# Kernel optimization log

Measured on AMD Instinct MI355X. Metric: run time of the kernel, lower is better.

## Reference

```python
import jax, jax.numpy as jnp
import numpy as np

B, C, H, W = 8, 256, 128, 128
WS, NH = 8, 8
HD = C // NH
HID = 4 * C
EPS = 1e-5


def _dwconv(x, w, b, pad):
    # x: [B,C,H,W], w: [C,1,k,k] depthwise
    y = jax.lax.conv_general_dilated(
        x, w, window_strides=(1, 1), padding=[(pad, pad), (pad, pad)],
        feature_group_count=C, dimension_numbers=('NCHW', 'OIHW', 'NCHW'))
    return y + b[None, :, None, None]


def _ln(x, g, b):
    m = jnp.mean(x, axis=-1, keepdims=True)
    v = jnp.mean(jnp.square(x - m), axis=-1, keepdims=True)
    return (x - m) * jax.lax.rsqrt(v + EPS) * g + b


def _mha(x, wqkv, bqkv, wo, bo):
    # x: [N,L,C]; torch nn.MultiheadAttention with q=k=v=x
    N, L, _ = x.shape
    qkv = x @ wqkv.T + bqkv
    q, k, v = jnp.split(qkv, 3, axis=-1)
    q = q.reshape(N, L, NH, HD)
    k = k.reshape(N, L, NH, HD)
    v = v.reshape(N, L, NH, HD)
    scale = HD ** -0.5
    a = jnp.einsum('nqhd,nkhd->nhqk', q * scale, k)
    a = jax.nn.softmax(a, axis=-1)
    o = jnp.einsum('nhqk,nkhd->nqhd', a, v).reshape(N, L, C)
    return o @ wo.T + bo


def _window_partition(x):
    b, c, h, w = x.shape
    x = x.reshape(b, c, h // WS, WS, w // WS, WS)
    return jnp.transpose(x, (0, 2, 4, 3, 5, 1)).reshape(-1, WS, WS, c)


def _window_reverse(win, h, w):
    c = win.shape[-1]
    x = win.reshape(-1, h // WS, w // WS, WS, WS, c)
    return jnp.transpose(x, (0, 5, 1, 3, 2, 4)).reshape(-1, c, h, w)


def _grid_partition(x):
    b, c, h, w = x.shape
    x = x.reshape(b, c, WS, h // WS, WS, w // WS)
    return jnp.transpose(x, (0, 3, 5, 2, 4, 1)).reshape(-1, WS, WS, c)


def _grid_reverse(grid, h, w):
    c = grid.shape[-1]
    x = grid.reshape(-1, h // WS, w // WS, WS, WS, c)
    return jnp.transpose(x, (0, 5, 2, 1, 3, 4)).reshape(-1, c, h, w)


def setup_inputs() -> dict:
    key = jax.random.key(0)
    ks = jax.random.split(key, 32)
    n = lambda k, s, sc=0.02: jax.random.normal(k, s, jnp.float32) * sc
    z = lambda s: jnp.zeros(s, jnp.float32)
    return {
        'x': jax.random.normal(ks[0], (B, C, H, W), jnp.float32),
        'w1': n(ks[1], (C, 1, 3, 3)), 'b1': z((C,)),
        'w2': n(ks[2], (C, 1, 5, 5)), 'b2': z((C,)),
        'w3': n(ks[3], (C, 1, 7, 7)), 'b3': z((C,)),
        'wf': n(ks[4], (C, 3 * C)), 'bf': z((C,)),
        'gw': jnp.ones((C,), jnp.float32), 'bw': z((C,)),
        'wqkv_w': n(ks[5], (3 * C, C)), 'bqkv_w': z((3 * C,)),
        'wo_w': n(ks[6], (C, C)), 'bo_w': z((C,)),
        'gg': jnp.ones((C,), jnp.float32), 'bg': z((C,)),
        'wqkv_g': n(ks[7], (3 * C, C)), 'bqkv_g': z((3 * C,)),
        'wo_g': n(ks[8], (C, C)), 'bo_g': z((C,)),
        'gm': jnp.ones((C,), jnp.float32), 'bm': z((C,)),
        'm1w': n(ks[9], (HID, C)), 'm1b': z((HID,)),
        'm2w': n(ks[10], (C, HID)), 'm2b': z((C,)),
    }


def reference(x, w1, b1, w2, b2, w3, b3, wf, bf, gw, bw, wqkv_w, bqkv_w, wo_w, bo_w,
              gg, bg, wqkv_g, bqkv_g, wo_g, bo_g, gm, bm, m1w, m1b, m2w, m2b):
    s1 = _dwconv(x, w1, b1, 1)
    s2 = _dwconv(x, w2, b2, 2)
    s3 = _dwconv(x, w3, b3, 3)
    cat = jnp.concatenate([s1, s2, s3], axis=1)  # [B,3C,H,W]
    x_multi = jnp.einsum('bkhw,ck->bchw', cat, wf) + bf[None, :, None, None]

    # window attention branch
    xw = _window_partition(x_multi).reshape(-1, WS * WS, C)
    xw = _ln(xw, gw, bw)
    xw = _mha(xw, wqkv_w, bqkv_w, wo_w, bo_w).reshape(-1, WS, WS, C)
    x = x + _window_reverse(xw, H, W)

    # grid attention branch
    xg = _grid_partition(x).reshape(-1, WS * WS, C)
    xg = _ln(xg, gg, bg)
    xg = _mha(xg, wqkv_g, bqkv_g, wo_g, bo_g).reshape(-1, WS, WS, C)
    x = x + _grid_reverse(xg, H, W)

    # MLP over flattened tokens
    xf = x.reshape(B, C, H * W).transpose(0, 2, 1)  # [B,HW,C]
    h = _ln(xf, gm, bm)
    h = jax.nn.gelu(h @ m1w.T + m1b, approximate=False)
    h = h @ m2w.T + m2b
    xf = xf + h
    return xf.transpose(0, 2, 1).reshape(B, C, H, W)
```

## Files before the change

### kernel.cpp

```cpp
#include <hip/hip_runtime.h>
#include <hip/hip_bf16.h>
#include <math.h>


#define CC 256
#define HH 128
#define WW 128
#define HWSZ 16384

typedef __attribute__((ext_vector_type(8))) short short8v;
typedef __attribute__((ext_vector_type(4))) float float4v;

#if defined(__has_builtin)
#if __has_builtin(__builtin_amdgcn_global_load_lds)
#define USE_GLDS 1
#endif
#endif
#ifndef USE_GLDS
#define USE_GLDS 0
#endif

static __device__ __forceinline__ float bf2f(unsigned short u) {
    union { float f; unsigned int i; } x; x.i = ((unsigned int)u) << 16; return x.f;
}
static __device__ __forceinline__ unsigned short f2bf(float f) {
    union { float f; unsigned int i; } x; x.f = f;
    unsigned int r = x.i + 0x7FFFu + ((x.i >> 16) & 1u);
    return (unsigned short)(r >> 16);
}
template<int FMT> static __device__ __forceinline__ float ldin(const void* p, size_t i) {
    if (FMT == 0) return bf2f(((const unsigned short*)p)[i]);
    return ((const float*)p)[i];
}

#if USE_GLDS
static __device__ __forceinline__ void gload16(const unsigned short* g, unsigned short* l) {
    __builtin_amdgcn_global_load_lds(
        (const __attribute__((address_space(1))) unsigned int*)g,
        (__attribute__((address_space(3))) unsigned int*)l, 16, 0, 0);
}
#endif

__global__ void probe_kernel(const unsigned short* x, int* flags) {
    __shared__ int mx[256];
    int m = 0;
    for (int i = threadIdx.x; i < 65536; i += 256) {
        int e = (x[i] >> 7) & 0xFF;
        m = m > e ? m : e;
    }
    mx[threadIdx.x] = m; __syncthreads();
    for (int s = 128; s > 0; s >>= 1) {
        if (threadIdx.x < s) mx[threadIdx.x] = mx[threadIdx.x] > mx[threadIdx.x + s] ? mx[threadIdx.x] : mx[threadIdx.x + s];
        __syncthreads();
    }
    if (threadIdx.x == 0) flags[0] = (mx[0] > 200) ? 1 : 0;
}
__global__ void report_ws_kernel(unsigned short* out, long long n, float code) {
    long long i = (long long)blockIdx.x * blockDim.x + threadIdx.x;
    const long long st = (long long)gridDim.x * blockDim.x;
    unsigned short c = f2bf(code);
    for (; i < n; i += st) out[i] = c;
}

#define WF_OFF   0
#define WQW_OFF  196608
#define WOW_OFF  393216
#define WQG_OFF  458752
#define WOG_OFF  655360
#define M1W_OFF  720896
#define M2W_OFF  983040
#define WTOT     1245184
#define BF_OFF   0
#define GW_OFF   256
#define BW_OFF   512
#define BQW_OFF  768
#define BOW_OFF  1536
#define GG_OFF   1792
#define BG_OFF   2048
#define BQG_OFF  2304
#define BOG_OFF  3072
#define GM_OFF   3328
#define BM_OFF   3584
#define M1B_OFF  3840
#define M2B_OFF  4864
#define BTOT     5120

template<int FMT>
__global__ __launch_bounds__(256) void convert_weights_kernel(
    const void* __restrict__ wf, const void* __restrict__ wqkv_w, const void* __restrict__ wo_w,
    const void* __restrict__ wqkv_g, const void* __restrict__ wo_g,
    const void* __restrict__ m1w, const void* __restrict__ m2w,
    unsigned short* __restrict__ out, const int* __restrict__ flags)
{
    if (flags[0] != FMT) return;
    int i = blockIdx.x * 256 + threadIdx.x;
    const int st = gridDim.x * 256;
    for (; i < WTOT; i += st) {
        const void* src; int off;
        if (i < WQW_OFF)      { src = wf;     off = i; }
        else if (i < WOW_OFF) { src = wqkv_w; off = i - WQW_OFF; }
        else if (i < WQG_OFF) { src = wo_w;   off = i - WOW_OFF; }
        else if (i < WOG_OFF) { src = wqkv_g; off = i - WQG_OFF; }
        else if (i < M1W_OFF) { src = wo_g;   off = i - WOG_OFF; }
        else if (i < M2W_OFF) { src = m1w;    off = i - M1W_OFF; }
        else                  { src = m2w;    off = i - M2W_OFF; }
        out[i] = (FMT == 0) ? ((const unsigned short*)src)[off]
                            : f2bf(((const float*)src)[off]);
    }
}

template<int FMT>
__global__ __launch_bounds__(256) void convert_bias_kernel(
    const void* bf_, const void* gw, const void* bw, const void* bqkv_w, const void* bo_w,
    const void* gg, const void* bg, const void* bqkv_g, const void* bo_g,
    const void* gm, const void* bm, const void* m1b, const void* m2b,
    float* __restrict__ out, const int* __restrict__ flags)
{
    if (flags[0] != FMT) return;
    int i = blockIdx.x * 256 + threadIdx.x;
    if (i >= BTOT) return;
    const void* src; int off;
    if (i < GW_OFF)        { src = bf_;    off = i; }
    else if (i < BW_OFF)   { src = gw;     off = i - GW_OFF; }
    else if (i < BQW_OFF)  { src = bw;     off = i - BW_OFF; }
    else if (i < BOW_OFF)  { src = bqkv_w; off = i - BQW_OFF; }
    else if (i < GG_OFF)   { src = bo_w;   off = i - BOW_OFF; }
    else if (i < BG_OFF)   { src = gg;     off = i - GG_OFF; }
    else if (i < BQG_OFF)  { src = bg;     off = i - BG_OFF; }
    else if (i < BOG_OFF)  { src = bqkv_g; off = i - BQG_OFF; }
    else if (i < GM_OFF)   { src = bo_g;   off = i - BOG_OFF; }
    else if (i < BM_OFF)   { src = gm;     off = i - GM_OFF; }
    else if (i < M1B_OFF)  { src = bm;     off = i - BM_OFF; }
    else if (i < M2B_OFF)  { src = m1b;    off = i - M1B_OFF; }
    else                   { src = m2b;    off = i - M2B_OFF; }
    out[i] = ldin<FMT>(src, off);
}

template<int FMT>
__global__ __launch_bounds__(256) void transpose_in_kernel(
    const void* __restrict__ in, float* __restrict__ out, const int* __restrict__ flags)
{
    if (flags[0] != FMT) return;
    __shared__ float tile[64][65];
    const int b  = blockIdx.z;
    const int s0 = blockIdx.x * 64;
    const int r0 = blockIdx.y * 64;
    const int tx = threadIdx.x & 63;
    const int ty = threadIdx.x >> 6;
    const size_t sb = (size_t)b * CC * HWSZ;
    float* dst = out + (size_t)b * HWSZ * CC;
#pragma unroll
    for (int rr = 0; rr < 16; ++rr) {
        int row = ty + rr * 4;
        tile[row][tx] = ldin<FMT>(in, sb + (size_t)(r0 + row) * HWSZ + s0 + tx);
    }
    __syncthreads();
#pragma unroll
    for (int rr = 0; rr < 16; ++rr) {
        int srow = ty + rr * 4;
        dst[(size_t)(s0 + srow) * CC + r0 + tx] = tile[tx][srow];
    }
}

template<int FMT>
__global__ __launch_bounds__(256) void transpose_out_kernel(
    const float* __restrict__ in, void* __restrict__ out, const int* __restrict__ flags)
{
    if (flags[0] != FMT) return;
    __shared__ float tile[64][65];
    const int b  = blockIdx.z;
    const int h0 = blockIdx.x * 64;
    const int c0 = blockIdx.y * 64;
    const int tx = threadIdx.x & 63;
    const int ty = threadIdx.x >> 6;
    const float* src = in + (size_t)b * HWSZ * CC;
    const size_t db = (size_t)b * CC * HWSZ;
#pragma unroll
    for (int rr = 0; rr < 16; ++rr) {
        int row = ty + rr * 4;
        tile[row][tx] = src[(size_t)(h0 + row) * CC + c0 + tx];
    }
    __syncthreads();
#pragma unroll
    for (int rr = 0; rr < 16; ++rr) {
        int crow = ty + rr * 4;
        size_t di = db + (size_t)(c0 + crow) * HWSZ + h0 + tx;
        float v = tile[tx][crow];
        if (FMT) ((float*)out)[di] = v;
        else ((unsigned short*)out)[di] = f2bf(v);
    }
}

template<int FMT>
__global__ __launch_bounds__(256) void dwconv_cat_kernel(
    const void* __restrict__ x,
    const void* __restrict__ w1, const void* __restrict__ b1,
    const void* __restrict__ w2, const void* __restrict__ b2,
    const void* __restrict__ w3, const void* __restrict__ b3,
    unsigned short* __restrict__ cat, int Mc, const int* __restrict__ flags)
{
    if (flags[0] != FMT) return;
    __shared__ float patch[8][136];
    __shared__ float wt[83];
    const int hb = blockIdx.x;
    const int c  = blockIdx.y;
    const int b  = blockIdx.z;
    const int tid = threadIdx.x;

    if (tid < 83) {
        float v;
        if (tid < 9)       v = ldin<FMT>(w1, c * 9 + tid);
        else if (tid < 34) v = ldin<FMT>(w2, c * 25 + (tid - 9));
        else               v = ldin<FMT>(w3, c * 49 + (tid - 34));
        wt[tid] = v;
    }
    const int h0 = hb * 2;
    const size_t xb = ((size_t)b * CC + c) * HWSZ;
    for (int i = tid; i < 8 * 136; i += 256) {
        int r = i / 136, col = i % 136;
        int gh = h0 - 3 + r, gw = col - 3;
        float v = 0.f;
        if (gh >= 0 && gh < HH && gw >= 0 && gw < WW) v = ldin<FMT>(x, xb + gh * WW + gw);
        patch[r][col] = v;
    }
    __syncthreads();

    const int w  = tid & 127;
    const int dh = tid >> 7;
    const int pr = dh + 3;
    float s1 = ldin<FMT>(b1, c), s2 = ldin<FMT>(b2, c), s3 = ldin<FMT>(b3, c);
#pragma unroll
    for (int dy = -1; dy <= 1; ++dy)
#pragma unroll
        for (int dx = -1; dx <= 1; ++dx)
            s1 += patch[pr + dy][w + 3 + dx] * wt[(dy + 1) * 3 + (dx + 1)];
#pragma unroll
    for (int dy = -2; dy <= 2; ++dy)
#pragma unroll
        for (int dx = -2; dx <= 2; ++dx)
            s2 += patch[pr + dy][w + 3 + dx] * wt[9 + (dy + 2) * 5 + (dx + 2)];
#pragma unroll
    for (int dy = -3; dy <= 3; ++dy)
#pragma unroll
        for (int dx = -3; dx <= 3; ++dx)
            s3 += patch[pr + dy][w + 3 + dx] * wt[34 + (dy + 3) * 7 + (dx + 3)];

    const size_t m = (size_t)b * HWSZ + (size_t)(h0 + dh) * WW + w;
    cat[(size_t)c * Mc + m]         = f2bf(s1);
    cat[(size_t)(256 + c) * Mc + m] = f2bf(s2);
    cat[(size_t)(512 + c) * Mc + m] = f2bf(s3);
}

template<int ALAYOUT, int EPI>
__global__ __launch_bounds__(256) void gemm_mfma_kernel(
    const unsigned short* __restrict__ A, const unsigned short* __restrict__ Bw,
    const float* __restrict__ bias, void* __restrict__ Cout,
    int N, int K, int lda)
{
    constexpr int ASTR = ALAYOUT ? 72 : 64;
    __shared__ unsigned short As[128 * ASTR];
    __shared__ unsigned short Bs[128 * 64];
    const int tid  = threadIdx.x;
    const int lane = tid & 63;
    const int wv   = tid >> 6;
    const int wm   = (wv >> 1) * 64;
    const int wn   = (wv & 1) * 64;
    const int l15  = lane & 15;
    const int quad = lane >> 4;

    const int nbx = gridDim.x;
    const int nwg = nbx * gridDim.y;
    const int bid = blockIdx.y * nbx + blockIdx.x;
    const int swz = (bid & 7) * (nwg >> 3) + (bid >> 3);
    const int m0 = (swz / nbx) * 128;
    const int n0 = (swz % nbx) * 128;

    const int sr   = lane >> 3;
    const int scol = (lane & 7) * 8;

    float4v acc[4][4] = {};

    for (int k0 = 0; k0 < K; k0 += 64) {
        __syncthreads();
        if (ALAYOUT == 0) {
            const unsigned short* ga = A + (size_t)(m0 + wv * 32 + sr) * K + k0 + scol;
#pragma unroll
            for (int p = 0; p < 4; ++p) {
                unsigned short* lb = &As[(wv * 32 + p * 8) * 64];
#if USE_GLDS
                gload16(ga + (size_t)(p * 8) * K, lb);
#else
                *(short8v*)(lb + lane * 8) = *(const short8v*)(ga + (size_t)(p * 8) * K);
#endif
            }
        } else {
#pragma unroll
            for (int p = 0; p < 4; ++p) {
                const int k  = p * 16 + (tid >> 4);
                const int mm = (tid & 15) * 8;
                const unsigned short* g = A + (size_t)(k0 + k) * lda + m0 + mm;
                ushort4 va = *(const ushort4*)g;
                ushort4 vb = *(const ushort4*)(g + 4);
                As[(mm + 0) * 72 + k] = va.x; As[(mm + 1) * 72 + k] = va.y;
                As[(mm + 2) * 72 + k] = va.z; As[(mm + 3) * 72 + k] = va.w;
                As[(mm + 4) * 72 + k] = vb.x; As[(mm + 5) * 72 + k] = vb.y;
                As[(mm + 6) * 72 + k] = vb.z; As[(mm + 7) * 72 + k] = vb.w;
            }
        }
        {
            const unsigned short* gb = Bw + (size_t)(n0 + wv * 32 + sr) * K + k0 + scol;
#pragma unroll
            for (int p = 0; p < 4; ++p) {
                unsigned short* lb = &Bs[(wv * 32 + p * 8) * 64];
#if USE_GLDS
                gload16(gb + (size_t)(p * 8) * K, lb);
#else
                *(short8v*)(lb + lane * 8) = *(const short8v*)(gb + (size_t)(p * 8) * K);
#endif
            }
        }
#if USE_GLDS
        asm volatile("s_waitcnt vmcnt(0)" ::: "memory");
#endif
        __syncthreads();

#pragma unroll
        for (int ks = 0; ks < 64; ks += 32) {
            short8v af[4], bfv[4];
#pragma unroll
            for (int i = 0; i < 4; ++i)
                af[i] = *(const short8v*)&As[(wm + i * 16 + l15) * ASTR + ks + quad * 8];
#pragma unroll
            for (int i = 0; i < 4; ++i)
                bfv[i] = *(const short8v*)&Bs[(wn + i * 16 + l15) * 64 + ks + quad * 8];
#pragma unroll
            for (int mi = 0; mi < 4; ++mi)
#pragma unroll
                for (int ni = 0; ni < 4; ++ni)
                    acc[mi][ni] = __builtin_amdgcn_mfma_f32_16x16x32_bf16(
                        af[mi], bfv[ni], acc[mi][ni], 0, 0, 0);
        }
    }

    float bv[4];
#pragma unroll
    for (int ni = 0; ni < 4; ++ni) bv[ni] = bias[n0 + wn + ni * 16 + l15];

#pragma unroll
    for (int mi = 0; mi < 4; ++mi) {
#pragma unroll
        for (int r = 0; r < 4; ++r) {
            const size_t row = (size_t)(m0 + wm + mi * 16 + quad * 4 + r);
#pragma unroll
            for (int ni = 0; ni < 4; ++ni) {
                const int col = n0 + wn + ni * 16 + l15;
                float v = acc[mi][ni][r] + bv[ni];
                if (EPI == 0) {
                    ((unsigned short*)Cout)[row * N + col] = f2bf(v);
                } else if (EPI == 1) {
                    float g = 0.5f * v * (1.0f + erff(v * 0.70710678118654752f));
                    ((unsigned short*)Cout)[row * N + col] = f2bf(g);
                } else {
                    ((float*)Cout)[row * N + col] += v;
                }
            }
        }
    }
}

template<int FIN>
__global__ __launch_bounds__(256) void ln_kernel(
    const void* __restrict__ inv, const float* __restrict__ g,
    const float* __restrict__ b, unsigned short* __restrict__ out)
{
    const int lane = threadIdx.x & 63;
    const int wv   = threadIdx.x >> 6;
    const size_t m = (size_t)blockIdx.x * 4 + wv;
    const int c0 = lane * 4;
    float v[4];
    if (FIN == 0) {
        ushort4 u = *(const ushort4*)((const unsigned short*)inv + m * CC + c0);
        v[0] = bf2f(u.x); v[1] = bf2f(u.y); v[2] = bf2f(u.z); v[3] = bf2f(u.w);
    } else {
        float4 f = *(const float4*)((const float*)inv + m * CC + c0);
        v[0] = f.x; v[1] = f.y; v[2] = f.z; v[3] = f.w;
    }
    float s  = v[0] + v[1] + v[2] + v[3];
    float sq = v[0]*v[0] + v[1]*v[1] + v[2]*v[2] + v[3]*v[3];
#pragma unroll
    for (int off = 32; off > 0; off >>= 1) {
        s  += __shfl_xor(s,  off);
        sq += __shfl_xor(sq, off);
    }
    const float mean = s * 0.00390625f;
    float var = sq * 0.00390625f - mean * mean;
    if (var < 0.f) var = 0.f;
    const float rs = rsqrtf(var + 1e-5f);
    ushort4 o;
    o.x = f2bf((v[0] - mean) * rs * g[c0 + 0] + b[c0 + 0]);
    o.y = f2bf((v[1] - mean) * rs * g[c0 + 1] + b[c0 + 1]);
    o.z = f2bf((v[2] - mean) * rs * g[c0 + 2] + b[c0 + 2]);
    o.w = f2bf((v[3] - mean) * rs * g[c0 + 3] + b[c0 + 3]);
    *(ushort4*)(out + m * CC + c0) = o;
}

template<int MODE>
__global__ __launch_bounds__(256) void attn_kernel(
    const unsigned short* __restrict__ qkv, unsigned short* __restrict__ attn_out)
{
    __shared__ float qs[64][36];
    __shared__ float ks[64][36];
    __shared__ float vs[64][36];
    __shared__ float S[64][68];
    const int tid = threadIdx.x;
    const int wi  = blockIdx.x;
    const int b   = wi >> 8;
    const int rem = wi & 255;
    const int i2  = rem >> 4;
    const int j2  = rem & 15;

    const int t  = tid >> 2;
    const int c8 = (tid & 3) * 8;
    const int p = t >> 3, qq = t & 7;
    int h_r, w_r, h_w, w_w;
    if (MODE == 0) {
        h_r = i2 * 8 + p;  w_r = j2 * 8 + qq;
        h_w = h_r;         w_w = w_r;
    } else {
        h_r = p * 16 + i2; w_r = qq * 16 + j2;
        h_w = j2 * 8 + (i2 >> 1);
        w_w = (i2 & 1) * 64 + p * 8 + qq;
    }
    const size_t gt_r = (size_t)b * HWSZ + (size_t)h_r * WW + w_r;
    const size_t gt_w = (size_t)b * HWSZ + (size_t)h_w * WW + w_w;

    const float scale = 0.17677669529663687f;
    const int ti = tid >> 4;
    const int tj = tid & 15;

    for (int head = 0; head < 8; ++head) {
        const unsigned short* base = qkv + gt_r * 768 + head * 32 + c8;
        ushort4 qa = *(const ushort4*)(base);
        ushort4 qb = *(const ushort4*)(base + 4);
        ushort4 ka = *(const ushort4*)(base + 256);
        ushort4 kb = *(const ushort4*)(base + 260);
        ushort4 va = *(const ushort4*)(base + 512);
        ushort4 vb = *(const ushort4*)(base + 516);
        qs[t][c8 + 0] = bf2f(qa.x) * scale; qs[t][c8 + 1] = bf2f(qa.y) * scale;
        qs[t][c8 + 2] = bf2f(qa.z) * scale; qs[t][c8 + 3] = bf2f(qa.w) * scale;
        qs[t][c8 + 4] = bf2f(qb.x) * scale; qs[t][c8 + 5] = bf2f(qb.y) * scale;
        qs[t][c8 + 6] = bf2f(qb.z) * scale; qs[t][c8 + 7] = bf2f(qb.w) * scale;
        ks[t][c8 + 0] = bf2f(ka.x); ks[t][c8 + 1] = bf2f(ka.y);
        ks[t][c8 + 2] = bf2f(ka.z); ks[t][c8 + 3] = bf2f(ka.w);
        ks[t][c8 + 4] = bf2f(kb.x); ks[t][c8 + 5] = bf2f(kb.y);
        ks[t][c8 + 6] = bf2f(kb.z); ks[t][c8 + 7] = bf2f(kb.w);
        vs[t][c8 + 0] = bf2f(va.x); vs[t][c8 + 1] = bf2f(va.y);
        vs[t][c8 + 2] = bf2f(va.z); vs[t][c8 + 3] = bf2f(va.w);
        vs[t][c8 + 4] = bf2f(vb.x); vs[t][c8 + 5] = bf2f(vb.y);
        vs[t][c8 + 6] = bf2f(vb.z); vs[t][c8 + 7] = bf2f(vb.w);
        __syncthreads();

        float sr[4][4] = {};
#pragma unroll 8
        for (int c = 0; c < 32; ++c) {
            float qv[4], kv[4];
#pragma unroll
            for (int i = 0; i < 4; ++i) qv[i] = qs[ti * 4 + i][c];
#pragma unroll
            for (int j = 0; j < 4; ++j) kv[j] = ks[tj * 4 + j][c];
#pragma unroll
            for (int i = 0; i < 4; ++i)
#pragma unroll
                for (int j = 0; j < 4; ++j)
                    sr[i][j] += qv[i] * kv[j];
        }
#pragma unroll
        for (int i = 0; i < 4; ++i)
#pragma unroll
            for (int j = 0; j < 4; ++j)
                S[ti * 4 + i][tj * 4 + j] = sr[i][j];
        __syncthreads();

        {
            const int r  = tid >> 2;
            const int s0 = (tid & 3) * 16;
            float mx = -1e30f;
#pragma unroll
            for (int j = 0; j < 16; ++j) mx = fmaxf(mx, S[r][s0 + j]);
            mx = fmaxf(mx, __shfl_xor(mx, 1));
            mx = fmaxf(mx, __shfl_xor(mx, 2));
            float sum = 0.f;
#pragma unroll
            for (int j = 0; j < 16; ++j) {
                float e = expf(S[r][s0 + j] - mx);
                S[r][s0 + j] = e;
                sum += e;
            }
            sum += __shfl_xor(sum, 1);
            sum += __shfl_xor(sum, 2);
            float inv = 1.f / sum;
#pragma unroll
            for (int j = 0; j < 16; ++j) S[r][s0 + j] *= inv;
        }
        __syncthreads();

        float ov[8] = {};
#pragma unroll 8
        for (int j = 0; j < 64; ++j) {
            float pv = S[t][j];
            const float4 v0 = *(const float4*)&vs[j][c8];
            const float4 v1 = *(const float4*)&vs[j][c8 + 4];
            ov[0] += pv * v0.x; ov[1] += pv * v0.y;
            ov[2] += pv * v0.z; ov[3] += pv * v0.w;
            ov[4] += pv * v1.x; ov[5] += pv * v1.y;
            ov[6] += pv * v1.z; ov[7] += pv * v1.w;
        }
        unsigned short* op = attn_out + gt_w * CC + head * 32 + c8;
        ushort4 o1, o2;
        o1.x = f2bf(ov[0]); o1.y = f2bf(ov[1]); o1.z = f2bf(ov[2]); o1.w = f2bf(ov[3]);
        o2.x = f2bf(ov[4]); o2.y = f2bf(ov[5]); o2.z = f2bf(ov[6]); o2.w = f2bf(ov[7]);
        *(ushort4*)op = o1;
        *(ushort4*)(op + 4) = o2;
        __syncthreads();
    }
}

extern "C" void kernel_launch(void* const* d_in, const int* in_sizes, int n_in,
                              void* d_out, int out_size, void* d_ws, size_t ws_size,
                              hipStream_t stream)
{
    const void* x      = d_in[0];
    const void* w1     = d_in[1];  const void* b1  = d_in[2];
    const void* w2     = d_in[3];  const void* b2  = d_in[4];
    const void* w3     = d_in[5];  const void* b3  = d_in[6];
    const void* wf     = d_in[7];  const void* bf_ = d_in[8];
    const void* gw     = d_in[9];  const void* bw  = d_in[10];
    const void* wqkv_w = d_in[11]; const void* bqkv_w = d_in[12];
    const void* wo_w   = d_in[13]; const void* bo_w   = d_in[14];
    const void* gg     = d_in[15]; const void* bg  = d_in[16];
    const void* wqkv_g = d_in[17]; const void* bqkv_g = d_in[18];
    const void* wo_g   = d_in[19]; const void* bo_g   = d_in[20];
    const void* gm     = d_in[21]; const void* bm  = d_in[22];
    const void* m1w    = d_in[23]; const void* m1b = d_in[24];
    const void* m2w    = d_in[25]; const void* m2b = d_in[26];

    const size_t MiB = 1048576ull;
    const long long nout = (long long)out_size;

    if (72 * MiB > ws_size) {
        float wsMiB = (float)(ws_size / MiB);
        if (wsMiB > 8192.f) wsMiB = 8192.f;
        report_ws_kernel<<<1024, 256, 0, stream>>>((unsigned short*)d_out, nout, 1024.f + wsMiB);
        return;
    }

    int nb = 8;
    while (nb > 1 && (size_t)nb * 64 * MiB + 8 * MiB > ws_size) nb >>= 1;
    const int nchunks = 8 / nb;
    const int Mc = nb * HWSZ;

    char* ws = (char*)d_ws;
    float*          xs   = (float*)ws;
    unsigned short* regA = (unsigned short*)(ws + (size_t)nb * 16 * MiB);
    unsigned short* xmat = (unsigned short*)(ws + (size_t)nb * 48 * MiB);
    unsigned short* xln  = (unsigned short*)(ws + (size_t)nb * 56 * MiB);
    int*            flags = (int*)(ws + (size_t)nb * 64 * MiB);
    unsigned short* wbf  = (unsigned short*)(ws + (size_t)nb * 64 * MiB + 1 * MiB);
    float*          bcv  = (float*)(ws + (size_t)nb * 64 * MiB + 4 * MiB);

    probe_kernel<<<1, 256, 0, stream>>>((const unsigned short*)x, flags);
    convert_weights_kernel<0><<<1024, 256, 0, stream>>>(wf, wqkv_w, wo_w, wqkv_g, wo_g, m1w, m2w, wbf, flags);
    convert_weights_kernel<1><<<1024, 256, 0, stream>>>(wf, wqkv_w, wo_w, wqkv_g, wo_g, m1w, m2w, wbf, flags);
    convert_bias_kernel<0><<<20, 256, 0, stream>>>(bf_, gw, bw, bqkv_w, bo_w, gg, bg, bqkv_g, bo_g, gm, bm, m1b, m2b, bcv, flags);
    convert_bias_kernel<1><<<20, 256, 0, stream>>>(bf_, gw, bw, bqkv_w, bo_w, gg, bg, bqkv_g, bo_g, gm, bm, m1b, m2b, bcv, flags);

    const int MB = Mc / 128;
    for (int c = 0; c < nchunks; ++c) {
        const size_t elemOff = (size_t)c * nb * CC * HWSZ;
        const void* xc0 = (const void*)((const unsigned short*)x + elemOff);
        const void* xc1 = (const void*)((const float*)x + elemOff);
        void* outc0 = (void*)((unsigned short*)d_out + elemOff);
        void* outc1 = (void*)((float*)d_out + elemOff);
        unsigned short* cat  = regA;
        unsigned short* qkvb = regA;
        unsigned short* h1   = regA;
        unsigned short* xm   = xmat;
        unsigned short* attn = xmat;

        transpose_in_kernel<0><<<dim3(256, 4, nb), 256, 0, stream>>>(xc0, xs, flags);
        transpose_in_kernel<1><<<dim3(256, 4, nb), 256, 0, stream>>>(xc1, xs, flags);

        dwconv_cat_kernel<0><<<dim3(64, 256, nb), 256, 0, stream>>>(xc0, w1, b1, w2, b2, w3, b3, cat, Mc, flags);
        dwconv_cat_kernel<1><<<dim3(64, 256, nb), 256, 0, stream>>>(xc1, w1, b1, w2, b2, w3, b3, cat, Mc, flags);

        gemm_mfma_kernel<1, 0><<<dim3(2, MB), 256, 0, stream>>>(cat, wbf + WF_OFF, bcv + BF_OFF, xm, 256, 768, Mc);

        ln_kernel<0><<<Mc / 4, 256, 0, stream>>>(xm, bcv + GW_OFF, bcv + BW_OFF, xln);
        gemm_mfma_kernel<0, 0><<<dim3(6, MB), 256, 0, stream>>>(xln, wbf + WQW_OFF, bcv + BQW_OFF, qkvb, 768, 256, 0);
        attn_kernel<0><<<nb * 256, 256, 0, stream>>>(qkvb, attn);
        gemm_mfma_kernel<0, 2><<<dim3(2, MB), 256, 0, stream>>>(attn, wbf + WOW_OFF, bcv + BOW_OFF, xs, 256, 256, 0);

        ln_kernel<1><<<Mc / 4, 256, 0, stream>>>(xs, bcv + GG_OFF, bcv + BG_OFF, xln);
        gemm_mfma_kernel<0, 0><<<dim3(6, MB), 256, 0, stream>>>(xln, wbf + WQG_OFF, bcv + BQG_OFF, qkvb, 768, 256, 0);
        attn_kernel<1><<<nb * 256, 256, 0, stream>>>(qkvb, attn);
        gemm_mfma_kernel<0, 2><<<dim3(2, MB), 256, 0, stream>>>(attn, wbf + WOG_OFF, bcv + BOG_OFF, xs, 256, 256, 0);

        ln_kernel<1><<<Mc / 4, 256, 0, stream>>>(xs, bcv + GM_OFF, bcv + BM_OFF, xln);
        gemm_mfma_kernel<0, 1><<<dim3(8, MB), 256, 0, stream>>>(xln, wbf + M1W_OFF, bcv + M1B_OFF, h1, 1024, 256, 0);
        gemm_mfma_kernel<0, 2><<<dim3(2, MB), 256, 0, stream>>>(h1, wbf + M2W_OFF, bcv + M2B_OFF, xs, 256, 1024, 0);

        transpose_out_kernel<0><<<dim3(256, 4, nb), 256, 0, stream>>>(xs, outc0, flags);
        transpose_out_kernel<1><<<dim3(256, 4, nb), 256, 0, stream>>>(xs, outc1, flags);
    }
}
```

Baseline: 2.103 ms.

## Use MFMA for window attention and enlarge depthwise-conv row tiles

The attention kernel moves from scalar fp32 dot products in LDS to bf16 MFMA 16x16x32 for both QK^T and PV. Softmax now runs in registers using cross-lane shuffles, and two heads are processed per 64-channel group load. The depthwise conv kernel now handles 8 rows per block instead of 2 and loads its halo patch with vectorized float4 reads, which cuts redundant halo traffic. The trade-off is that probabilities and V go through bf16 rounding, and the conv block uses more LDS.

Result: faster. 1.842 ms (-12.4%).

```diff
diff --git a/kernel.cpp b/kernel.cpp
--- a/kernel.cpp
+++ b/kernel.cpp
@@ -200,7 +200,7 @@
     unsigned short* __restrict__ cat, int Mc, const int* __restrict__ flags)
 {
     if (flags[0] != FMT) return;
-    __shared__ float patch[8][136];
+    __shared__ float patch[14][140];
     __shared__ float wt[83];
     const int hb = blockIdx.x;
     const int c  = blockIdx.y;
@@ -214,41 +214,65 @@
         else               v = ldin<FMT>(w3, c * 49 + (tid - 34));
         wt[tid] = v;
     }
-    const int h0 = hb * 2;
+    const int h0 = hb * 8;
     const size_t xb = ((size_t)b * CC + c) * HWSZ;
-    for (int i = tid; i < 8 * 136; i += 256) {
-        int r = i / 136, col = i % 136;
-        int gh = h0 - 3 + r, gw = col - 3;
+
+    for (int i = tid; i < 448; i += 256) {
+        const int r  = i >> 5;
+        const int c4 = (i & 31) * 4;
+        const int gh = h0 - 3 + r;
+        float4 vv;
+        if (gh >= 0 && gh < HH) {
+            if (FMT == 0) {
+                ushort4 u = *(const ushort4*)((const unsigned short*)x + xb + (size_t)gh * WW + c4);
+                vv.x = bf2f(u.x); vv.y = bf2f(u.y); vv.z = bf2f(u.z); vv.w = bf2f(u.w);
+            } else {
+                vv = *(const float4*)((const float*)x + xb + (size_t)gh * WW + c4);
+            }
+        } else { vv.x = vv.y = vv.z = vv.w = 0.f; }
+        *(float4*)&patch[r][c4 + 4] = vv;
+    }
+    for (int i = tid; i < 84; i += 256) {
+        const int r = i / 6, j = i % 6;
+        const int gh = h0 - 3 + r;
+        const int gw = (j < 3) ? (j - 3) : (125 + j);
         float v = 0.f;
-        if (gh >= 0 && gh < HH && gw >= 0 && gw < WW) v = ldin<FMT>(x, xb + gh * WW + gw);
-        patch[r][col] = v;
+        if (gh >= 0 && gh < HH && gw >= 0 && gw < WW)
+            v = ldin<FMT>(x, xb + (size_t)gh * WW + gw);
+        patch[r][gw + 4] = v;
     }
     __syncthreads();
 
     const int w  = tid & 127;
-    const int dh = tid >> 7;
-    const int pr = dh + 3;
-    float s1 = ldin<FMT>(b1, c), s2 = ldin<FMT>(b2, c), s3 = ldin<FMT>(b3, c);
-#pragma unroll
-    for (int dy = -1; dy <= 1; ++dy)
-#pragma unroll
-        for (int dx = -1; dx <= 1; ++dx)
-            s1 += patch[pr + dy][w + 3 + dx] * wt[(dy + 1) * 3 + (dx + 1)];
-#pragma unroll
-    for (int dy = -2; dy <= 2; ++dy)
-#pragma unroll
-        for (int dx = -2; dx <= 2; ++dx)
-            s2 += patch[pr + dy][w + 3 + dx] * wt[9 + (dy + 2) * 5 + (dx + 2)];
-#pragma unroll
-    for (int dy = -3; dy <= 3; ++dy)
-#pragma unroll
-        for (int dx = -3; dx <= 3; ++dx)
-            s3 += patch[pr + dy][w + 3 + dx] * wt[34 + (dy + 3) * 7 + (dx + 3)];
-
-    const size_t m = (size_t)b * HWSZ + (size_t)(h0 + dh) * WW + w;
-    cat[(size_t)c * Mc + m]         = f2bf(s1);
-    cat[(size_t)(256 + c) * Mc + m] = f2bf(s2);
-    cat[(size_t)(512 + c) * Mc + m] = f2bf(s3);
+    const int rb = (tid >> 7) * 4;
+    const float bb1 = ldin<FMT>(b1, c), bb2 = ldin<FMT>(b2, c), bb3 = ldin<FMT>(b3, c);
+
+#pragma unroll
+    for (int ri = 0; ri < 4; ++ri) {
+        const int row = rb + ri;
+        const int pr  = row + 3;
+        float s1 = bb1, s2 = bb2, s3 = bb3;
+#pragma unroll
+        for (int dy = -1; dy <= 1; ++dy)
+#pragma unroll
+            for (int dx = -1; dx <= 1; ++dx)
+                s1 += patch[pr + dy][w + 4 + dx] * wt[(dy + 1) * 3 + (dx + 1)];
+#pragma unroll
+        for (int dy = -2; dy <= 2; ++dy)
+#pragma unroll
+            for (int dx = -2; dx <= 2; ++dx)
+                s2 += patch[pr + dy][w + 4 + dx] * wt[9 + (dy + 2) * 5 + (dx + 2)];
+#pragma unroll
+        for (int dy = -3; dy <= 3; ++dy)
+#pragma unroll
+            for (int dx = -3; dx <= 3; ++dx)
+                s3 += patch[pr + dy][w + 4 + dx] * wt[34 + (dy + 3) * 7 + (dx + 3)];
+
+        const size_t m = (size_t)b * HWSZ + (size_t)(h0 + row) * WW + w;
+        cat[(size_t)c * Mc + m]         = f2bf(s1);
+        cat[(size_t)(256 + c) * Mc + m] = f2bf(s2);
+        cat[(size_t)(512 + c) * Mc + m] = f2bf(s3);
+    }
 }
 
 template<int ALAYOUT, int EPI>
@@ -408,120 +432,119 @@
 __global__ __launch_bounds__(256) void attn_kernel(
     const unsigned short* __restrict__ qkv, unsigned short* __restrict__ attn_out)
 {
-    __shared__ float qs[64][36];
-    __shared__ float ks[64][36];
-    __shared__ float vs[64][36];
-    __shared__ float S[64][68];
-    const int tid = threadIdx.x;
-    const int wi  = blockIdx.x;
-    const int b   = wi >> 8;
-    const int rem = wi & 255;
-    const int i2  = rem >> 4;
-    const int j2  = rem & 15;
-
-    const int t  = tid >> 2;
-    const int c8 = (tid & 3) * 8;
-    const int p = t >> 3, qq = t & 7;
-    int h_r, w_r, h_w, w_w;
-    if (MODE == 0) {
-        h_r = i2 * 8 + p;  w_r = j2 * 8 + qq;
-        h_w = h_r;         w_w = w_r;
-    } else {
-        h_r = p * 16 + i2; w_r = qq * 16 + j2;
-        h_w = j2 * 8 + (i2 >> 1);
-        w_w = (i2 & 1) * 64 + p * 8 + qq;
-    }
-    const size_t gt_r = (size_t)b * HWSZ + (size_t)h_r * WW + w_r;
-    const size_t gt_w = (size_t)b * HWSZ + (size_t)h_w * WW + w_w;
+    __shared__ unsigned short q_lds[64 * 72];
+    __shared__ unsigned short k_lds[64 * 72];
+    __shared__ unsigned short v_lds[64 * 72];
+    __shared__ unsigned short vt_lds[32 * 72];
+    __shared__ unsigned short p_lds[64 * 72];
+
+    const int tid  = threadIdx.x;
+    const int lane = tid & 63;
+    const int wv   = tid >> 6;
+    const int l15  = lane & 15;
+    const int quad = lane >> 4;
+    const int wi   = blockIdx.x;
+    const int b    = wi >> 8;
+    const int rem  = wi & 255;
+    const int i2   = rem >> 4;
+    const int j2   = rem & 15;
 
     const float scale = 0.17677669529663687f;
-    const int ti = tid >> 4;
-    const int tj = tid & 15;
-
-    for (int head = 0; head < 8; ++head) {
-        const unsigned short* base = qkv + gt_r * 768 + head * 32 + c8;
-        ushort4 qa = *(const ushort4*)(base);
-        ushort4 qb = *(const ushort4*)(base + 4);
-        ushort4 ka = *(const ushort4*)(base + 256);
-        ushort4 kb = *(const ushort4*)(base + 260);
-        ushort4 va = *(const ushort4*)(base + 512);
-        ushort4 vb = *(const ushort4*)(base + 516);
-        qs[t][c8 + 0] = bf2f(qa.x) * scale; qs[t][c8 + 1] = bf2f(qa.y) * scale;
-        qs[t][c8 + 2] = bf2f(qa.z) * scale; qs[t][c8 + 3] = bf2f(qa.w) * scale;
-        qs[t][c8 + 4] = bf2f(qb.x) * scale; qs[t][c8 + 5] = bf2f(qb.y) * scale;
-        qs[t][c8 + 6] = bf2f(qb.z) * scale; qs[t][c8 + 7] = bf2f(qb.w) * scale;
-        ks[t][c8 + 0] = bf2f(ka.x); ks[t][c8 + 1] = bf2f(ka.y);
-        ks[t][c8 + 2] = bf2f(ka.z); ks[t][c8 + 3] = bf2f(ka.w);
-        ks[t][c8 + 4] = bf2f(kb.x); ks[t][c8 + 5] = bf2f(kb.y);
-        ks[t][c8 + 6] = bf2f(kb.z); ks[t][c8 + 7] = bf2f(kb.w);
-        vs[t][c8 + 0] = bf2f(va.x); vs[t][c8 + 1] = bf2f(va.y);
-        vs[t][c8 + 2] = bf2f(va.z); vs[t][c8 + 3] = bf2f(va.w);
-        vs[t][c8 + 4] = bf2f(vb.x); vs[t][c8 + 5] = bf2f(vb.y);
-        vs[t][c8 + 6] = bf2f(vb.z); vs[t][c8 + 7] = bf2f(vb.w);
-        __syncthreads();
-
-        float sr[4][4] = {};
-#pragma unroll 8
-        for (int c = 0; c < 32; ++c) {
-            float qv[4], kv[4];
-#pragma unroll
-            for (int i = 0; i < 4; ++i) qv[i] = qs[ti * 4 + i][c];
-#pragma unroll
-            for (int j = 0; j < 4; ++j) kv[j] = ks[tj * 4 + j][c];
-#pragma unroll
-            for (int i = 0; i < 4; ++i)
-#pragma unroll
-                for (int j = 0; j < 4; ++j)
-                    sr[i][j] += qv[i] * kv[j];
-        }
-#pragma unroll
-        for (int i = 0; i < 4; ++i)
-#pragma unroll
-            for (int j = 0; j < 4; ++j)
-                S[ti * 4 + i][tj * 4 + j] = sr[i][j];
-        __syncthreads();
-
-        {
-            const int r  = tid >> 2;
-            const int s0 = (tid & 3) * 16;
-            float mx = -1e30f;
-#pragma unroll
-            for (int j = 0; j < 16; ++j) mx = fmaxf(mx, S[r][s0 + j]);
-            mx = fmaxf(mx, __shfl_xor(mx, 1));
-            mx = fmaxf(mx, __shfl_xor(mx, 2));
-            float sum = 0.f;
-#pragma unroll
-            for (int j = 0; j < 16; ++j) {
-                float e = expf(S[r][s0 + j] - mx);
-                S[r][s0 + j] = e;
-                sum += e;
-            }
-            sum += __shfl_xor(sum, 1);
-            sum += __shfl_xor(sum, 2);
-            float inv = 1.f / sum;
-#pragma unroll
-            for (int j = 0; j < 16; ++j) S[r][s0 + j] *= inv;
+
+    auto gt_read = [&](int tok) -> size_t {
+        const int p = tok >> 3, qq = tok & 7;
+        int h_r, w_r;
+        if (MODE == 0) { h_r = i2 * 8 + p;  w_r = j2 * 8 + qq; }
+        else           { h_r = p * 16 + i2; w_r = qq * 16 + j2; }
+        return (size_t)b * HWSZ + (size_t)h_r * WW + w_r;
+    };
+    auto gt_write = [&](int tok) -> size_t {
+        const int p = tok >> 3, qq = tok & 7;
+        int h_w, w_w;
+        if (MODE == 0) { h_w = i2 * 8 + p; w_w = j2 * 8 + qq; }
+        else { h_w = j2 * 8 + (i2 >> 1); w_w = (i2 & 1) * 64 + p * 8 + qq; }
+        return (size_t)b * HWSZ + (size_t)h_w * WW + w_w;
+    };
+
+    for (int g = 0; g < 4; ++g) {
+        for (int v = tid; v < 512; v += 256) {
+            const int tok = v >> 3;
+            const int cg  = (v & 7) * 8;
+            const unsigned short* src = qkv + gt_read(tok) * 768 + g * 64 + cg;
+            *(short8v*)&q_lds[tok * 72 + cg] = *(const short8v*)(src);
+            *(short8v*)&k_lds[tok * 72 + cg] = *(const short8v*)(src + 256);
+            *(short8v*)&v_lds[tok * 72 + cg] = *(const short8v*)(src + 512);
         }
         __syncthreads();
 
-        float ov[8] = {};
-#pragma unroll 8
-        for (int j = 0; j < 64; ++j) {
-            float pv = S[t][j];
-            const float4 v0 = *(const float4*)&vs[j][c8];
-            const float4 v1 = *(const float4*)&vs[j][c8 + 4];
-            ov[0] += pv * v0.x; ov[1] += pv * v0.y;
-            ov[2] += pv * v0.z; ov[3] += pv * v0.w;
-            ov[4] += pv * v1.x; ov[5] += pv * v1.y;
-            ov[6] += pv * v1.z; ov[7] += pv * v1.w;
+#pragma unroll
+        for (int hl = 0; hl < 2; ++hl) {
+            {
+                const int tok = lane;
+                const int dg  = wv * 8;
+                short8v vv = *(const short8v*)&v_lds[tok * 72 + hl * 32 + dg];
+#pragma unroll
+                for (int j = 0; j < 8; ++j)
+                    vt_lds[(dg + j) * 72 + tok] = (unsigned short)vv[j];
+            }
+
+            short8v af = *(const short8v*)&q_lds[(16 * wv + l15) * 72 + hl * 32 + quad * 8];
+            float4v s[4];
+#pragma unroll
+            for (int ni = 0; ni < 4; ++ni) {
+                short8v bfv = *(const short8v*)&k_lds[(16 * ni + l15) * 72 + hl * 32 + quad * 8];
+                float4v z = {};
+                s[ni] = __builtin_amdgcn_mfma_f32_16x16x32_bf16(af, bfv, z, 0, 0, 0);
+            }
+
+#pragma unroll
+            for (int r = 0; r < 4; ++r) {
+                float m1 = fmaxf(fmaxf(s[0][r], s[1][r]), fmaxf(s[2][r], s[3][r]));
+#pragma unroll
+                for (int off = 1; off < 16; off <<= 1) m1 = fmaxf(m1, __shfl_xor(m1, off));
+                const float rowmax = m1 * scale;
+                float sum = 0.f;
+#pragma unroll
+                for (int ni = 0; ni < 4; ++ni) {
+                    const float e = __expf(s[ni][r] * scale - rowmax);
+                    s[ni][r] = e; sum += e;
+                }
+#pragma unroll
+                for (int off = 1; off < 16; off <<= 1) sum += __shfl_xor(sum, off);
+                const float inv = 1.f / sum;
+#pragma unroll
+                for (int ni = 0; ni < 4; ++ni) s[ni][r] *= inv;
+            }
+
+#pragma unroll
+            for (int ni = 0; ni < 4; ++ni)
+#pragma unroll
+                for (int r = 0; r < 4; ++r)
+                    p_lds[(16 * wv + quad * 4 + r) * 72 + ni * 16 + l15] = f2bf(s[ni][r]);
+
+            __syncthreads();
+
+            float4v o[2] = {};
+#pragma unroll
+            for (int kk = 0; kk < 2; ++kk) {
+                short8v pf = *(const short8v*)&p_lds[(16 * wv + l15) * 72 + kk * 32 + quad * 8];
+#pragma unroll
+                for (int dt = 0; dt < 2; ++dt) {
+                    short8v vf = *(const short8v*)&vt_lds[(dt * 16 + l15) * 72 + kk * 32 + quad * 8];
+                    o[dt] = __builtin_amdgcn_mfma_f32_16x16x32_bf16(pf, vf, o[dt], 0, 0, 0);
+                }
+            }
+
+            const int head = g * 2 + hl;
+#pragma unroll
+            for (int r = 0; r < 4; ++r) {
+                const int tok = 16 * wv + quad * 4 + r;
+                unsigned short* op = attn_out + gt_write(tok) * CC + head * 32;
+                op[l15]      = f2bf(o[0][r]);
+                op[16 + l15] = f2bf(o[1][r]);
+            }
+            __syncthreads();
         }
-        unsigned short* op = attn_out + gt_w * CC + head * 32 + c8;
-        ushort4 o1, o2;
-        o1.x = f2bf(ov[0]); o1.y = f2bf(ov[1]); o1.z = f2bf(ov[2]); o1.w = f2bf(ov[3]);
-        o2.x = f2bf(ov[4]); o2.y = f2bf(ov[5]); o2.z = f2bf(ov[6]); o2.w = f2bf(ov[7]);
-        *(ushort4*)op = o1;
-        *(ushort4*)(op + 4) = o2;
-        __syncthreads();
     }
 }
 
@@ -590,8 +613,8 @@
         transpose_in_kernel<0><<<dim3(256, 4, nb), 256, 0, stream>>>(xc0, xs, flags);
         transpose_in_kernel<1><<<dim3(256, 4, nb), 256, 0, stream>>>(xc1, xs, flags);
 
-        dwconv_cat_kernel<0><<<dim3(64, 256, nb), 256, 0, stream>>>(xc0, w1, b1, w2, b2, w3, b3, cat, Mc, flags);
-        dwconv_cat_kernel<1><<<dim3(64, 256, nb), 256, 0, stream>>>(xc1, w1, b1, w2, b2, w3, b3, cat, Mc, flags);
+        dwconv_cat_kernel<0><<<dim3(16, 256, nb), 256, 0, stream>>>(xc0, w1, b1, w2, b2, w3, b3, cat, Mc, flags);
+        dwconv_cat_kernel<1><<<dim3(16, 256, nb), 256, 0, stream>>>(xc1, w1, b1, w2, b2, w3, b3, cat, Mc, flags);
 
         gemm_mfma_kernel<1, 0><<<dim3(2, MB), 256, 0, stream>>>(cat, wbf + WF_OFF, bcv + BF_OFF, xm, 256, 768, Mc);
 
```
